# Kernel tuning notes

Hardware: AMD Instinct MI355X
Metric: run time of the kernel (lower is better)

Reference implementation:

```python
import jax, jax.numpy as jnp
import numpy as np

GRID_MIN = -2.0
GRID_MAX = 2.0
NUM_GRIDS = 8
IN_DIM = 512
OUT_DIM = 512
N = 16384
SPLINE_SCALE = 0.1


def setup_inputs() -> dict:
    key = jax.random.key(0)
    k_x, k_sw, k_w, k_b = jax.random.split(key, 4)
    x = jax.random.normal(k_x, (N, IN_DIM), dtype=jnp.float32)
    grid = jnp.linspace(GRID_MIN, GRID_MAX, NUM_GRIDS, dtype=jnp.float32)
    spline_weight = jax.random.normal(k_sw, (IN_DIM * NUM_GRIDS, OUT_DIM), dtype=jnp.float32) * SPLINE_SCALE
    bound = 1.0 / np.sqrt(IN_DIM)
    base_w = jax.random.uniform(k_w, (OUT_DIM, IN_DIM), minval=-bound, maxval=bound, dtype=jnp.float32)
    base_b = jax.random.uniform(k_b, (OUT_DIM,), minval=-bound, maxval=bound, dtype=jnp.float32)
    return {"x": x, "grid": grid, "spline_weight": spline_weight, "base_w": base_w, "base_b": base_b}


def reference(x, grid, spline_weight, base_w, base_b):
    # Gaussian RBF basis over the grid: (N, in_dim, num_grids)
    h = (GRID_MAX - GRID_MIN) / (NUM_GRIDS - 1)  # grid spacing
    basis = jnp.exp(-(((x[..., None] - grid) / h) ** 2))
    ret = basis.reshape(x.shape[0], -1) @ spline_weight  # (N, out_dim)
    base = jax.nn.silu(x) @ base_w.T + base_b
    return ret + base
```

## Files before the change

### kernel.cpp

```cpp
#include <hip/hip_runtime.h>
#include <hip/hip_bf16.h>

typedef __attribute__((ext_vector_type(8))) short short8;
typedef __attribute__((ext_vector_type(4))) float floatx4;

#define N_ROWS   16384
#define IN_DIM   512
#define OUT_DIM  512
#define K_SPLINE 4096
#define K_TOT    4608
#define NPER     36
#define NSPER    32
#define NKTILE   144
#define ROWS_B   128
#define COLS_B   256
#define L2E      1.4426950408889634f
#define C2E      0.13533528323661270f

__device__ __forceinline__ unsigned short f2bf(float f) {
    unsigned int u = __float_as_uint(f);
    unsigned int r = u + 0x7FFFu + ((u >> 16) & 1u);
    return (unsigned short)(r >> 16);
}

__device__ __forceinline__ unsigned packtrunc(float f0, float f1) {
    return __builtin_amdgcn_perm(__float_as_uint(f1), __float_as_uint(f0), 0x07060302);
}

__global__ __launch_bounds__(256) void prep_kernel(
    const float* __restrict__ sw, const float* __restrict__ bw,
    unsigned short* __restrict__ Btf)
{
    const int t     = threadIdx.x;
    const int lane  = t & 63;
    const int kt32  = blockIdx.x * 4 + (t >> 6);
    const int ct    = blockIdx.y;
    const int mn    = lane & 15, q = lane >> 4;
    const int n     = ct * 16 + mn;
    const int kbase = kt32 * 32 + q * 8;
    short8 v;
    if (kbase < K_SPLINE) {
        #pragma unroll
        for (int j = 0; j < 8; ++j)
            v[j] = (short)f2bf(sw[(size_t)(kbase + j) * OUT_DIM + n]);
    } else {
        #pragma unroll
        for (int j = 0; j < 8; ++j)
            v[j] = (short)f2bf(bw[(size_t)n * IN_DIM + (kbase + j - K_SPLINE)]);
    }
    reinterpret_cast<short8*>(Btf)[(size_t)(ct * NKTILE + kt32) * 64 + lane] = v;
}

__device__ __forceinline__ uint4 basis_pack(float X) {
    const float u = fmaf(1.75f, X, 3.5f);
    float b = __builtin_amdgcn_exp2f(-(u * u) * L2E);
    float r = __builtin_amdgcn_exp2f(fmaf(2.0f * L2E, u, -L2E));
    float v[8];
    v[0] = b;
    #pragma unroll
    for (int j = 1; j < 8; ++j) { b *= r; r *= C2E; v[j] = b; }
    uint4 p;
    p.x = packtrunc(v[0], v[1]);
    p.y = packtrunc(v[2], v[3]);
    p.z = packtrunc(v[4], v[5]);
    p.w = packtrunc(v[6], v[7]);
    return p;
}

__device__ __forceinline__ void stageA128(unsigned short* dst, const float* xrow,
                                          int rowA, int colq, int p, float4 xsp)
{
    unsigned short* arow = dst + rowA * 128;
    if (p < NSPER) {
        const float xv[4] = {xsp.x, xsp.y, xsp.z, xsp.w};
        #pragma unroll
        for (int e = 0; e < 4; ++e) {
            const uint4 pk = basis_pack(xv[e]);
            const int blk = (colq * 4 + e) ^ (rowA & 15);
            *reinterpret_cast<uint4*>(arow + blk * 8) = pk;
        }
    } else {
        const float* xs = xrow + (p - NSPER) * 128 + colq * 32;
        #pragma unroll
        for (int e = 0; e < 4; ++e) {
            const float4 a0 = *reinterpret_cast<const float4*>(xs + e * 8);
            const float4 a1 = *reinterpret_cast<const float4*>(xs + e * 8 + 4);
            const float f[8] = {a0.x, a0.y, a0.z, a0.w, a1.x, a1.y, a1.z, a1.w};
            float s[8];
            #pragma unroll
            for (int j = 0; j < 8; ++j)
                s[j] = f[j] * __builtin_amdgcn_rcpf(
                    1.0f + __builtin_amdgcn_exp2f(-f[j] * L2E));
            uint4 pk;
            pk.x = packtrunc(s[0], s[1]);
            pk.y = packtrunc(s[2], s[3]);
            pk.z = packtrunc(s[4], s[5]);
            pk.w = packtrunc(s[6], s[7]);
            const int blk = (colq * 4 + e) ^ (rowA & 15);
            *reinterpret_cast<uint4*>(arow + blk * 8) = pk;
        }
    }
}

template<bool PREP>
__device__ __forceinline__ void load_b(short8 bb[4][2], const short8* __restrict__ Bf,
                                       const size_t* bbase, int p, int kh,
                                       const float* __restrict__ sw,
                                       const float* __restrict__ bw,
                                       int col0, int lane)
{
    if (PREP) {
        #pragma unroll
        for (int nt = 0; nt < 4; ++nt)
            #pragma unroll
            for (int s = 0; s < 2; ++s)
                bb[nt][s] = Bf[bbase[nt] + (size_t)(p * 4 + kh * 2 + s) * 64];
    } else {
        const int mn = lane & 15, q = lane >> 4;
        #pragma unroll
        for (int nt = 0; nt < 4; ++nt) {
            const int n = col0 + nt * 16 + mn;
            #pragma unroll
            for (int s = 0; s < 2; ++s) {
                short8 v;
                #pragma unroll
                for (int j = 0; j < 8; ++j) {
                    const int k = (p * 4 + kh * 2 + s) * 32 + q * 8 + j;
                    const float val = (k < K_SPLINE)
                        ? sw[(size_t)k * OUT_DIM + n]
                        : bw[(size_t)n * IN_DIM + (k - K_SPLINE)];
                    v[j] = (short)f2bf(val);
                }
                bb[nt][s] = v;
            }
        }
    }
}

template<bool PREP>
__global__ __launch_bounds__(512, 2) void kan_kernel(
    const float* __restrict__ x,
    const unsigned short* __restrict__ Btf,
    const float* __restrict__ sw,
    const float* __restrict__ bw,
    const float* __restrict__ bias,
    float* __restrict__ out)
{
    __shared__ unsigned short Als[2][ROWS_B * 128];

    const int tid  = threadIdx.x;
    const int w    = tid >> 6;
    const int lane = tid & 63;
    const int kh   = w >> 2;
    const int wc   = w & 3;
    const int q    = lane >> 4;
    const int mn   = lane & 15;
    const int bid  = blockIdx.x;
    const int row0 = (bid >> 1) * ROWS_B;
    const int col0 = (bid & 1) * COLS_B + wc * 64;

    const int rowA = tid >> 2;
    const int colq = tid & 3;
    const float* xrow = x + (size_t)(row0 + rowA) * IN_DIM;

    size_t bbase[4];
    #pragma unroll
    for (int nt = 0; nt < 4; ++nt)
        bbase[nt] = (size_t)(((col0 >> 4) + nt) * NKTILE) * 64 + lane;
    const short8* Bf = reinterpret_cast<const short8*>(Btf);

    floatx4 acc[8][4];
    #pragma unroll
    for (int i = 0; i < 8; ++i)
        #pragma unroll
        for (int j = 0; j < 4; ++j)
            acc[i][j] = (floatx4){0.f, 0.f, 0.f, 0.f};

    short8 bb[4][2];

    float4 xsp = *reinterpret_cast<const float4*>(xrow + colq * 4);
    stageA128(&Als[0][0], xrow, rowA, colq, 0, xsp);
    xsp = *reinterpret_cast<const float4*>(xrow + 16 + colq * 4);
    __syncthreads();

    for (int p = 0; p < NPER; ++p) {
        const unsigned short* Acur = &Als[p & 1][0];

        load_b<PREP>(bb, Bf, bbase, p, kh, sw, bw, col0, lane);

        if (p + 1 < NPER) {
            stageA128(&Als[(p & 1) ^ 1][0], xrow, rowA, colq, p + 1, xsp);
            if (p + 2 < NSPER)
                xsp = *reinterpret_cast<const float4*>(
                    xrow + (p + 2) * 16 + colq * 4);
        }

        #pragma unroll
        for (int s = 0; s < 2; ++s) {
            const int st = kh * 2 + s;
            short8 af[8];
            #pragma unroll
            for (int mt = 0; mt < 8; ++mt) {
                const int r = mt * 16 + mn;
                af[mt] = *reinterpret_cast<const short8*>(
                    Acur + r * 128 + (((st * 4 + q) ^ (r & 15)) * 8));
            }
            __builtin_amdgcn_s_setprio(1);
            #pragma unroll
            for (int mt = 0; mt < 8; ++mt)
                #pragma unroll
                for (int nt = 0; nt < 4; ++nt)
                    acc[mt][nt] = __builtin_amdgcn_mfma_f32_16x16x32_bf16(
                        af[mt], bb[nt][s], acc[mt][nt], 0, 0, 0);
            __builtin_amdgcn_s_setprio(0);
        }
        __syncthreads();
    }

    floatx4* ex = reinterpret_cast<floatx4*>(&Als[0][0]);
    if (kh) {
        #pragma unroll
        for (int m = 0; m < 4; ++m)
            #pragma unroll
            for (int nt = 0; nt < 4; ++nt)
                ex[((wc * 4 + m) * 4 + nt) * 64 + lane] = acc[m][nt];
    }
    __syncthreads();
    if (!kh) {
        #pragma unroll
        for (int nt = 0; nt < 4; ++nt) {
            const int col = col0 + nt * 16 + mn;
            const float bv = bias[col];
            #pragma unroll
            for (int m = 0; m < 4; ++m) {
                const floatx4 o  = acc[m][nt];
                const floatx4 r2 = ex[((wc * 4 + m) * 4 + nt) * 64 + lane];
                const int rb = row0 + m * 16 + q * 4;
                #pragma unroll
                for (int e = 0; e < 4; ++e)
                    out[(size_t)(rb + e) * OUT_DIM + col] = o[e] + r2[e] + bv;
            }
        }
    }
    __syncthreads();
    if (!kh) {
        #pragma unroll
        for (int m = 0; m < 4; ++m)
            #pragma unroll
            for (int nt = 0; nt < 4; ++nt)
                ex[((wc * 4 + m) * 4 + nt) * 64 + lane] = acc[4 + m][nt];
    }
    __syncthreads();
    if (kh) {
        #pragma unroll
        for (int nt = 0; nt < 4; ++nt) {
            const int col = col0 + nt * 16 + mn;
            const float bv = bias[col];
            #pragma unroll
            for (int m = 0; m < 4; ++m) {
                const floatx4 o  = acc[4 + m][nt];
                const floatx4 r2 = ex[((wc * 4 + m) * 4 + nt) * 64 + lane];
                const int rb = row0 + (4 + m) * 16 + q * 4;
                #pragma unroll
                for (int e = 0; e < 4; ++e)
                    out[(size_t)(rb + e) * OUT_DIM + col] = o[e] + r2[e] + bv;
            }
        }
    }
}

extern "C" void kernel_launch(void* const* d_in, const int* in_sizes, int n_in,
                              void* d_out, int out_size, void* d_ws, size_t ws_size,
                              hipStream_t stream)
{
    const float* x    = (const float*)d_in[0];
    const float* sw   = (const float*)d_in[2];
    const float* bw   = (const float*)d_in[3];
    const float* bias = (const float*)d_in[4];
    float* out = (float*)d_out;

    const int nblk = (N_ROWS / ROWS_B) * (OUT_DIM / COLS_B);
    const size_t bt_bytes = (size_t)OUT_DIM * K_TOT * sizeof(unsigned short);
    if (ws_size >= bt_bytes) {
        unsigned short* Btf = (unsigned short*)d_ws;
        prep_kernel<<<dim3(NKTILE / 4, OUT_DIM / 16), 256, 0, stream>>>(sw, bw, Btf);
        kan_kernel<true><<<dim3(nblk), 512, 0, stream>>>(
            x, Btf, sw, bw, bias, out);
    } else {
        kan_kernel<false><<<dim3(nblk), 512, 0, stream>>>(
            x, nullptr, sw, bw, bias, out);
    }
}
```

Measured before the change: 163.2 us.

## Double-buffer B fragments in registers and prefetch next K-step ahead of MFMAs

Loads the B fragments for step p+1 into a second register set while step p computes, by unrolling the K loop by two and ping-ponging both the A LDS buffers and the B register buffers. Each k-step's A fragment reads are split into two groups of four row tiles so fewer A registers are live at once. The __syncthreads is replaced with an explicit lgkmcnt(0) wait plus s_barrier, so the barrier does not wait on outstanding global loads. The aim is to hide global-load latency of B behind MFMA work, at the cost of extra VGPRs that could spill or reduce occupancy.

Result: slower. 253.4 us (+55.2%).

```diff
diff --git a/kernel.cpp b/kernel.cpp
--- a/kernel.cpp
+++ b/kernel.cpp
@@ -25,6 +25,10 @@
 
 __device__ __forceinline__ unsigned packtrunc(float f0, float f1) {
     return __builtin_amdgcn_perm(__float_as_uint(f1), __float_as_uint(f0), 0x07060302);
+}
+
+__device__ __forceinline__ void barrier_lgkm() {
+    asm volatile("s_waitcnt lgkmcnt(0)\n\ts_barrier" ::: "memory");
 }
 
 __global__ __launch_bounds__(256) void prep_kernel(
@@ -103,7 +107,7 @@
 }
 
 template<bool PREP>
-__device__ __forceinline__ void load_b(short8 bb[4][2], const short8* __restrict__ Bf,
+__device__ __forceinline__ void load_b(short8 (&bb)[4][2], const short8* __restrict__ Bf,
                                        const size_t* bbase, int p, int kh,
                                        const float* __restrict__ sw,
                                        const float* __restrict__ bw,
@@ -176,45 +180,52 @@
         for (int j = 0; j < 4; ++j)
             acc[i][j] = (floatx4){0.f, 0.f, 0.f, 0.f};
 
-    short8 bb[4][2];
+    short8 bbA[4][2], bbB[4][2];
 
     float4 xsp = *reinterpret_cast<const float4*>(xrow + colq * 4);
+    load_b<PREP>(bbA, Bf, bbase, 0, kh, sw, bw, col0, lane);
     stageA128(&Als[0][0], xrow, rowA, colq, 0, xsp);
     xsp = *reinterpret_cast<const float4*>(xrow + 16 + colq * 4);
     __syncthreads();
 
-    for (int p = 0; p < NPER; ++p) {
-        const unsigned short* Acur = &Als[p & 1][0];
-
-        load_b<PREP>(bb, Bf, bbase, p, kh, sw, bw, col0, lane);
-
+    auto body = [&](int p, const unsigned short* Acur, unsigned short* Anxt,
+                    short8 (&bbu)[4][2], short8 (&bbl)[4][2]) {
         if (p + 1 < NPER) {
-            stageA128(&Als[(p & 1) ^ 1][0], xrow, rowA, colq, p + 1, xsp);
+            load_b<PREP>(bbl, Bf, bbase, p + 1, kh, sw, bw, col0, lane);
+            stageA128(Anxt, xrow, rowA, colq, p + 1, xsp);
             if (p + 2 < NSPER)
                 xsp = *reinterpret_cast<const float4*>(
                     xrow + (p + 2) * 16 + colq * 4);
         }
-
         #pragma unroll
         for (int s = 0; s < 2; ++s) {
             const int st = kh * 2 + s;
-            short8 af[8];
-            #pragma unroll
-            for (int mt = 0; mt < 8; ++mt) {
-                const int r = mt * 16 + mn;
-                af[mt] = *reinterpret_cast<const short8*>(
-                    Acur + r * 128 + (((st * 4 + q) ^ (r & 15)) * 8));
+            #pragma unroll
+            for (int mg = 0; mg < 2; ++mg) {
+                short8 af[4];
+                #pragma unroll
+                for (int mt = 0; mt < 4; ++mt) {
+                    const int r = (mg * 4 + mt) * 16 + mn;
+                    af[mt] = *reinterpret_cast<const short8*>(
+                        Acur + r * 128 + (((st * 4 + q) ^ (r & 15)) * 8));
+                }
+                __builtin_amdgcn_s_setprio(1);
+                #pragma unroll
+                for (int mt = 0; mt < 4; ++mt)
+                    #pragma unroll
+                    for (int nt = 0; nt < 4; ++nt)
+                        acc[mg * 4 + mt][nt] = __builtin_amdgcn_mfma_f32_16x16x32_bf16(
+                            af[mt], bbu[nt][s], acc[mg * 4 + mt][nt], 0, 0, 0);
+                __builtin_amdgcn_s_setprio(0);
             }
-            __builtin_amdgcn_s_setprio(1);
-            #pragma unroll
-            for (int mt = 0; mt < 8; ++mt)
-                #pragma unroll
-                for (int nt = 0; nt < 4; ++nt)
-                    acc[mt][nt] = __builtin_amdgcn_mfma_f32_16x16x32_bf16(
-                        af[mt], bb[nt][s], acc[mt][nt], 0, 0, 0);
-            __builtin_amdgcn_s_setprio(0);
-        }
-        __syncthreads();
+        }
+        barrier_lgkm();
+    };
+
+    #pragma unroll 1
+    for (int p = 0; p < NPER; p += 2) {
+        body(p,     &Als[0][0], &Als[1][0], bbA, bbB);
+        body(p + 1, &Als[1][0], &Als[0][0], bbB, bbA);
     }
 
     floatx4* ex = reinterpret_cast<floatx4*>(&Als[0][0]);
```
